# Optimization experiments

Hardware: AMD Instinct MI355X
Metric: run time of the kernel (lower is better)

## Reference

```python
import jax, jax.numpy as jnp
import numpy as np
from math import ceil

N, C_IN, HV, WV = 4, 3, 256, 256
C, K, NUM_LAYERS = 16, 3, 10
HK, WK = 45, 45
PROX_SCALE, KSCALE, KBSCALE, EPS = 10.0, 100.0, 0.01, 1e-8


def conv2_same(x, w):
    # torch F.conv2d (cross-correlation) with 'same' padding
    return jax.lax.conv_general_dilated(x, w, (1, 1), 'SAME',
                                        dimension_numbers=('NCHW', 'OIHW', 'NCHW'))


def pad_to(x, size):
    h, w = x.shape[-2], x.shape[-1]
    pads = [(0, 0)] * (x.ndim - 2) + [(0, size[0] - h), (0, size[1] - w)]
    return jnp.pad(x, pads)


def soft_threshold(x, b):
    return jnp.sign(x) * jax.nn.relu(jnp.abs(x) - b)


def circ_shift(x, s):
    return jnp.roll(x, (-s[0], -s[1]), axis=(-2, -1))


def csq(c):
    return (c * jnp.conj(c)).real


def forward(blurred_image, w0, ws, biases, kernel_biases, kernel_proxes, zetas, eta):
    Nb, C_in, Hv, Wv = blurred_image.shape
    Hs, Ws = Hv + HK - 1, Wv + WK - 1
    Hb, Wb = Hs + HK - 1, Ws + WK - 1
    fft_size = (int(ceil(Hb / 64.0) * 64), int(ceil(Wb / 64.0) * 64))
    rfft = lambda x: jnp.fft.rfft2(x, s=fft_size, axes=(-2, -1))
    irfft = lambda X: jnp.fft.irfft2(X, s=fft_size, axes=(-2, -1))

    # first-layer filter: zero-mean per (out,in) filter, then spatial reflect
    w_mean = w0.reshape(C, C_in, -1).mean(axis=-1)
    w0c = w0 - w_mean[:, :, None, None]
    w0_unreflected = jnp.transpose(w0c, (1, 0, 2, 3))   # (C_in, C, K, K)
    w0r = w0c[:, :, ::-1, ::-1]

    # analysis: cascade of convs, each feature stack padded to fft_size
    wy_list = []
    fy = blurred_image
    for layer in range(NUM_LAYERS):
        w = w0r if layer == 0 else ws[layer - 1]
        fy = conv2_same(fy, w)
        fy_p = pad_to(jnp.pad(fy, ((0, 0), (0, 0), (HK - 1, HK - 1), (WK - 1, WK - 1))), fft_size)
        wy_list.append(fy_p)

    delta = jnp.zeros((Nb, HK, WK), dtype=blurred_image.dtype).at[:, HK // 2, WK // 2].set(1.0)
    b0 = biases[0][None, :, None, None]
    z = soft_threshold(circ_shift(wy_list[-1], (HK // 2, WK // 2)), b0)
    Fz = rfft(z)
    k = delta
    Fg = None
    for layer in range(NUM_LAYERS):
        fy_p = wy_list.pop()
        Ffy = rfft(fy_p)                       # (N, C, H, Wf) complex
        Fk = rfft(k)[:, None]                  # (N, 1, H, Wf)
        zeta = PROX_SCALE * zetas[layer][None, :, None, None]
        num = zeta * (jnp.conj(Fk) * Ffy) + Fz
        den = zeta * csq(Fk) + 1.0
        Fg = num / (den + EPS)
        b = biases[layer + 1][None, :, None, None]
        z = soft_threshold(irfft(Fg), b)
        Fz = rfft(z)
        zk = kernel_proxes[layer]
        num_k = zk * jnp.sum(jnp.conj(Fz) * Ffy, axis=1) + Fk[:, 0]
        den_k = zk * jnp.sum(csq(Fz), axis=1) + 1.0
        k = irfft(num_k / (den_k + EPS))
        k_flat = k.reshape(Nb, -1)
        k_max = jax.scipy.special.logsumexp(k_flat * KSCALE, axis=-1) / KSCALE
        bk = KBSCALE * kernel_biases[layer]
        k = jax.nn.relu(k[:, :HK, :WK] - bk * k_max[:, None, None])
        k_sum = jnp.sum(k, axis=(1, 2), keepdims=True)
        k = (k + EPS * delta) / (k_sum + EPS)

    # final closed-form image solve in frequency domain (3-channel Cramer's rule)
    Fy = rfft(jnp.pad(blurred_image, ((0, 0), (0, 0), (HK - 1, HK - 1), (WK - 1, WK - 1))))
    Fk = rfft(k)                                # (N, H, Wf)
    Fw0 = rfft(circ_shift(pad_to(w0_unreflected, fft_size), (K // 2, K // 2)))  # (C_in, C, H, Wf)
    b_final = biases[NUM_LAYERS + 1][None, :, None, None]
    Fg = rfft(soft_threshold(irfft(Fg), b_final))

    eta_s = PROX_SCALE * eta[None, :, None, None]      # (1, C, 1, 1)
    Fwr, Fwg, Fwb = Fw0[0:1], Fw0[1:2], Fw0[2:3]       # (1, C, H, Wf)
    Fyr, Fyg, Fyb = Fy[:, 0], Fy[:, 1], Fy[:, 2]
    Fk_sq = csq(Fk)
    Crr = Fk_sq + jnp.sum(eta_s * csq(Fwr), axis=1)
    Cgg = Fk_sq + jnp.sum(eta_s * csq(Fwg), axis=1)
    Cbb = Fk_sq + jnp.sum(eta_s * csq(Fwb), axis=1)
    Crg = jnp.sum(eta_s * jnp.conj(Fwr) * Fwg, axis=1)
    Crb = jnp.sum(eta_s * jnp.conj(Fwr) * Fwb, axis=1)
    Cgb = jnp.sum(eta_s * jnp.conj(Fwg) * Fwb, axis=1)
    Fk_conj = jnp.conj(Fk)
    Br = Fk_conj * Fyr + jnp.sum(eta_s * jnp.conj(Fwr) * Fg, axis=1)
    Bg = Fk_conj * Fyg + jnp.sum(eta_s * jnp.conj(Fwg) * Fg, axis=1)
    Bb = Fk_conj * Fyb + jnp.sum(eta_s * jnp.conj(Fwb) * Fg, axis=1)
    Crg_sq, Crb_sq, Cgb_sq = csq(Crg), csq(Crb), csq(Cgb)
    Irr = Cgg * Cbb - Cgb_sq
    Igg = Crr * Cbb - Crb_sq
    Ibb = Crr * Cgg - Crg_sq
    Irg = jnp.conj(Cgb) * Crb - Cbb * Crg
    Irb = Crg * Cgb - Cgg * Crb
    Igb = jnp.conj(Crg) * Crb - Crr * Cgb
    den = (Crr * (Cgg * Cbb - Cgb_sq) - Cgg * Crb_sq - Cbb * Crg_sq
           + 2 * (Crg * Cgb * jnp.conj(Crb)).real) + EPS
    Fxr = Irr * Br + Irg * Bg + Irb * Bb
    Fxg = jnp.conj(Irg) * Br + Igg * Bg + Igb * Bb
    Fxb = jnp.conj(Irb) * Br + jnp.conj(Igb) * Bg + Ibb * Bb
    Fx = jnp.stack([Fxr, Fxg, Fxb], axis=1) / den[:, None]

    image = irfft(Fx)[:, :, HK // 2:HK // 2 + Hv, WK // 2:WK // 2 + Wv]
    return image, k


def setup_inputs() -> dict:
    key = jax.random.key(0)
    ks = jax.random.split(key, 4)

    def xavier(k, shape, fan_in, fan_out):
        std = (2.0 / (fan_in + fan_out)) ** 0.5
        return std * jax.random.normal(k, shape, dtype=jnp.float32)

    return {
        'blurred_image': jax.random.normal(ks[0], (N, C_IN, HV, WV), dtype=jnp.float32),
        'w0': xavier(ks[1], (C, C_IN, K, K), C_IN * K * K, C * K * K),
        'ws': xavier(ks[2], (NUM_LAYERS - 1, C, C, 3, 3), C * 9, C * 9),
        'biases': jnp.full((NUM_LAYERS + 2, C), 0.02, dtype=jnp.float32),
        'kernel_biases': jnp.zeros((NUM_LAYERS,), dtype=jnp.float32),
        'kernel_proxes': jnp.ones((NUM_LAYERS,), dtype=jnp.float32),
        'zetas': jnp.ones((NUM_LAYERS, C), dtype=jnp.float32),
        'eta': jnp.ones((C,), dtype=jnp.float32),
    }


def reference(blurred_image, w0, ws, biases, kernel_biases, kernel_proxes, zetas, eta):
    return forward(blurred_image, w0, ws, biases, kernel_biases, kernel_proxes, zetas, eta)
```

## Files before the change

kernel.cpp:

```cpp
#include <hip/hip_runtime.h>
#include <math.h>

#define FH 384
#define KF 193
#define KS 384
#define SPW 147456

typedef __attribute__((ext_vector_type(8))) short short8;
typedef __attribute__((ext_vector_type(4))) float f32x4;
typedef unsigned int u32;
typedef unsigned short u16;

static __device__ __forceinline__ float softt(float v, float b) {
    return copysignf(fmaxf(fabsf(v) - b, 0.f), v);
}
static __device__ __forceinline__ u16 bf16_rn(float v) {
    u32 u = __float_as_uint(v);
    u32 r = (u + 0x7FFFu + ((u >> 16) & 1u)) >> 16;
    return (u16)r;
}
static __device__ __forceinline__ float bf16_to_f(u16 h) {
    return __uint_as_float(((u32)h) << 16);
}
static __device__ __forceinline__ float2 ldc(const uint2* __restrict__ S, size_t i) {
    uint2 u = S[i];
    float2 r;
    r.x = __uint_as_float((u.x & 0xffffu) << 16) + __uint_as_float((u.y & 0xffffu) << 16);
    r.y = __uint_as_float(u.x & 0xffff0000u) + __uint_as_float(u.y & 0xffff0000u);
    return r;
}
static __device__ __forceinline__ uint2 packc(float re, float im) {
    u16 hr = bf16_rn(re), hi = bf16_rn(im);
    u16 lr = bf16_rn(re - bf16_to_f(hr)), li = bf16_rn(im - bf16_to_f(hi));
    uint2 o; o.x = (u32)hr | ((u32)hi << 16); o.y = (u32)lr | ((u32)li << 16);
    return o;
}

__global__ void init_ef_k(float2* Ef) {
    int idx = blockIdx.x * 256 + threadIdx.x;
    if (idx >= FH * FH) return;
    int h = idx / FH, j = idx % FH;
    int m = (h * j) % FH;
    float th = (float)(6.283185307179586 / FH) * (float)m;
    float2 v; v.x = cosf(th); v.y = -sinf(th);
    Ef[idx] = v;
}

__global__ void init_tw(float2* twT) {
    int i = blockIdx.x * 256 + threadIdx.x;
    if (i < 193) {
        float th = (float)(6.283185307179586 / 384.0) * (float)i;
        float2 v; v.x = cosf(th); v.y = sinf(th);
        twT[i] = v;
    }
}

__global__ void init_estack192(u16* __restrict__ H, u16* __restrict__ L, int inv)
{
    int idx = blockIdx.x * 256 + threadIdx.x;
    if (idx >= KS * KS) return;
    int gm = idx / KS, kp = idx % KS;
    int m = gm >> 1, comp = gm & 1;
    int t = kp >> 1, ri = kp & 1;
    int mm = (m * t) % 192;
    float th = (float)(6.283185307179586 / 192.0) * (float)mm;
    float c = cosf(th), s = sinf(th);
    float er, ei;
    if (inv) { er = c * (1.f/384.f); ei = s * (1.f/384.f); }
    else     { er = c;               ei = -s; }
    float v;
    if (comp == 0) v = (ri == 0) ? er : -ei;
    else           v = (ri == 0) ? ei :  er;
    u16 h = bf16_rn(v);
    H[idx] = h;
    L[idx] = bf16_rn(v - bf16_to_f(h));
}

__global__ void init_t192(u16* __restrict__ H, u16* __restrict__ L)
{
    int idx = blockIdx.x * 256 + threadIdx.x;
    if (idx >= 208 * 192) return;
    int n = idx / 192, m = idx % 192;
    float v = 0.f;
    if (n < 194) {
        int j = n >> 1, ri = n & 1;
        int mm = (j * m) % 192;
        float th = (float)(6.283185307179586 / 192.0) * (float)mm;
        v = ri ? -sinf(th) : cosf(th);
    }
    u16 h = bf16_rn(v);
    H[idx] = h;
    L[idx] = bf16_rn(v - bf16_to_f(h));
}

__global__ void init_u192(u16* __restrict__ H, u16* __restrict__ L)
{
    int idx = blockIdx.x * 256 + threadIdx.x;
    if (idx >= 192 * 224) return;
    int m = idx / 224, kk = idx % 224;
    float v = 0.f;
    if (kk < 194) {
        int j = kk >> 1, ri = kk & 1;
        float cj = (j == 0 || j == 96) ? (1.f/384.f) : (2.f/384.f);
        int mm = (j * m) % 192;
        float th = (float)(6.283185307179586 / 192.0) * (float)mm;
        v = ri ? -cj*sinf(th) : cj*cosf(th);
    }
    u16 h = bf16_rn(v);
// ... 249 lines not shown
#pragma unroll
    for (int mi = 0; mi < 2; ++mi)
#pragma unroll
        for (int nj = 0; nj < 4; ++nj) {
            accA[mi][nj] = (f32x4){0.f,0.f,0.f,0.f};
            accB[mi][nj] = (f32x4){0.f,0.f,0.f,0.f};
        }
    const u16* hP = Hs + (size_t)plane*inH*inW;
    const u16* lP = Ls + (size_t)plane*inH*inW;
    int W2  = inW >> 1;
    int ox2 = offX >> 1;
    bool al16 = ((ox2 & 7) == 0);
    int mhi = (offX + inW) >> 1;
    for (int kt = 0; kt < mhi; kt += 32) {
#pragma unroll
        for (int s = 0; s < 4; ++s) {
            int slot = tid + s*256;
            int p    = slot >> 9;
            int inr  = slot & 511;
            int r = inr >> 2, kq2 = inr & 3;
            int yy = y0 + r - offY;
            int m0 = kt + kq2*8;
            int pos = m0 - ox2;
            uint4 hq = {0u,0u,0u,0u}, lq4 = {0u,0u,0u,0u};
            if (yy >= 0 && yy < inH) {
                const u16* hr = hP + (size_t)yy*inW + (size_t)p*W2;
                const u16* lr = lP + (size_t)yy*inW + (size_t)p*W2;
                if (pos >= 0 && pos + 8 <= W2) {
                    if (al16) {
                        hq  = *(const uint4*)(hr + pos);
                        lq4 = *(const uint4*)(lr + pos);
                    } else {
                        hq.x = *(const u32*)(hr+pos);   hq.y = *(const u32*)(hr+pos+2);
                        hq.z = *(const u32*)(hr+pos+4); hq.w = *(const u32*)(hr+pos+6);
                        lq4.x = *(const u32*)(lr+pos);   lq4.y = *(const u32*)(lr+pos+2);
                        lq4.z = *(const u32*)(lr+pos+4); lq4.w = *(const u32*)(lr+pos+6);
                    }
                } else if (pos + 8 > 0 && pos < W2) {
#pragma unroll
                    for (int q = 0; q < 4; ++q) {
                        int pp = pos + 2*q;
                        if (pp >= 0 && pp + 2 <= W2) {
                            ((u32*)&hq)[q]  = *(const u32*)(hr+pp);
                            ((u32*)&lq4)[q] = *(const u32*)(lr+pp);
                        }
                    }
                }
            }
            int base = ((r >> 4)*64 + (r & 15) + 16*kq2)*8;
            *(uint4*)&AhS[p][base] = hq;
            *(uint4*)&AlS[p][base] = lq4;
        }
        __syncthreads();
        short8 A0h[2], A0l[2], A1h[2], A1l[2];
#pragma unroll
        for (int mi = 0; mi < 2; ++mi) {
            int fo = ((wave*2 + mi)*64 + lane)*8;
            A0h[mi] = *(const short8*)&AhS[0][fo];
            A0l[mi] = *(const short8*)&AlS[0][fo];
            A1h[mi] = *(const short8*)&AhS[1][fo];
            A1l[mi] = *(const short8*)&AlS[1][fo];
        }
#pragma unroll
        for (int nj = 0; nj < 4; ++nj) {
            if (nj >= njN) continue;
            size_t toff = (size_t)(col0 + nj*16 + lm)*192 + kt + lq*8;
            short8 Bh = *(const short8*)(TH + toff);
            short8 Bl = *(const short8*)(TL + toff);
#pragma unroll
            for (int mi = 0; mi < 2; ++mi) {
                accA[mi][nj] = __builtin_amdgcn_mfma_f32_16x16x32_bf16(A0h[mi], Bh, accA[mi][nj], 0, 0, 0);
                accA[mi][nj] = __builtin_amdgcn_mfma_f32_16x16x32_bf16(A0h[mi], Bl, accA[mi][nj], 0, 0, 0);
                accA[mi][nj] = __builtin_amdgcn_mfma_f32_16x16x32_bf16(A0l[mi], Bh, accA[mi][nj], 0, 0, 0);
                accB[mi][nj] = __builtin_amdgcn_mfma_f32_16x16x32_bf16(A1h[mi], Bh, accB[mi][nj], 0, 0, 0);
                accB[mi][nj] = __builtin_amdgcn_mfma_f32_16x16x32_bf16(A1h[mi], Bl, accB[mi][nj], 0, 0, 0);
                accB[mi][nj] = __builtin_amdgcn_mfma_f32_16x16x32_bf16(A1l[mi], Bh, accB[mi][nj], 0, 0, 0);
            }
        }
        __syncthreads();
    }
    r2c192_epilogue(accA, accB, col0, njN, y0, wave, lm, lq, twT, outp, B, plane);
}

__global__ void gpm_kernel(uint2* __restrict__ S, const float2* __restrict__ twT, int rows)
{
    int idx = blockIdx.x*256 + threadIdx.x;
    if (idx >= rows * 97) return;
    int j = idx % 97;
    size_t b = (size_t)(idx / 97) * KF;
    if (j == 96) {
        float2 f = ldc(S, b + 96);
        S[b + 96] = packc(2.f*f.x, -2.f*f.y);
    } else {
        float2 f1 = ldc(S, b + j);
        float2 f2 = ldc(S, b + 192 - j);
        float gpx = f1.x + f2.x, gpy = f1.y - f2.y;
        float hx  = f1.x - f2.x, hy  = f1.y + f2.y;
        float2 tw = twT[j];
        float gmx = tw.x*hx - tw.y*hy;
        float gmy = tw.x*hy + tw.y*hx;
        S[b + j]       = packc(gpx, gpy);
        S[b + 192 - j] = packc(gmx, gmy);
    }
}

__global__ __launch_bounds__(256) void c2r192(
    const uint2* __restrict__ Ain,
    const u16* __restrict__ UH, const u16* __restrict__ UL,
    float* __restrict__ outp, const float* __restrict__ thr,
    u16* __restrict__ spH, u16* __restrict__ spL, int B)
{
    __shared__ u16 AhS[2][8*64*8];
    __shared__ u16 AlS[2][8*64*8];
    int col0 = blockIdx.x * 64;
    int y0   = blockIdx.y * 128;
    int plane = blockIdx.z;
    int tid = threadIdx.x;
    int wave = tid >> 6, lane = tid & 63;
    int lm = lane & 15, lq = lane >> 4;
    f32x4 accP[2][4], accQ[2][4];
#pragma unroll
    for (int mi = 0; mi < 2; ++mi)
#pragma unroll
        for (int nj = 0; nj < 4; ++nj) {
            accP[mi][nj] = (f32x4){0.f,0.f,0.f,0.f};
            accQ[mi][nj] = (f32x4){0.f,0.f,0.f,0.f};
        }
    for (int kt = 0; kt < 194; kt += 32) {
#pragma unroll
        for (int s = 0; s < 8; ++s) {
            int slot = tid + s*256;
            int p   = slot >> 10;
            int inr = slot & 1023;
            int r = inr >> 3, kq = inr & 7;
            size_t rowb = ((size_t)(y0 + r)*B + plane)*KF;
            int j0 = (kt + kq*4) >> 1;
            uint2 u0, u1;
            u0.x = u0.y = u1.x = u1.y = 0u;
            if (p == 0) {
                if (j0 < 96) u0 = Ain[rowb + j0];
                else if (j0 == 96) {
                    uint2 t = Ain[rowb + 96];
                    u0.x = t.x & 0xffffu; u0.y = t.y & 0xffffu;
                }
                if (j0 + 1 < 96) u1 = Ain[rowb + j0 + 1];
            } else {
                if (j0 < 96) u0 = Ain[rowb + 192 - j0];
                else if (j0 == 96) {
                    uint2 t = Ain[rowb + 96];
                    u0.x = t.x >> 16; u0.y = t.y >> 16;
                }
                if (j0 + 1 < 96) u1 = Ain[rowb + 191 - j0];
            }
            int base = ((r >> 4)*64 + (r & 15) + 16*(kq >> 1))*8 + (kq & 1)*4;
            uint2 hp, lp;
            hp.x = u0.x; hp.y = u1.x;
            lp.x = u0.y; lp.y = u1.y;
            *(uint2*)&AhS[p][base] = hp;
            *(uint2*)&AlS[p][base] = lp;
        }
        __syncthreads();
        short8 A0h[2], A0l[2], A1h[2], A1l[2];
#pragma unroll
        for (int mi = 0; mi < 2; ++mi) {
            int fo = ((wave*2 + mi)*64 + lane)*8;
            A0h[mi] = *(const short8*)&AhS[0][fo];
            A0l[mi] = *(const short8*)&AlS[0][fo];
            A1h[mi] = *(const short8*)&AhS[1][fo];
            A1l[mi] = *(const short8*)&AlS[1][fo];
        }
#pragma unroll
        for (int nj = 0; nj < 4; ++nj) {
            size_t toff = (size_t)(col0 + nj*16 + lm)*224 + kt + lq*8;
            short8 Bh = *(const short8*)(UH + toff);
            short8 Bl = *(const short8*)(UL + toff);
#pragma unroll
            for (int mi = 0; mi < 2; ++mi) {
                accP[mi][nj] = __builtin_amdgcn_mfma_f32_16x16x32_bf16(A0h[mi], Bh, accP[mi][nj], 0, 0, 0);
                accP[mi][nj] = __builtin_amdgcn_mfma_f32_16x16x32_bf16(A0h[mi], Bl, accP[mi][nj], 0, 0, 0);
                accP[mi][nj] = __builtin_amdgcn_mfma_f32_16x16x32_bf16(A0l[mi], Bh, accP[mi][nj], 0, 0, 0);
                accQ[mi][nj] = __builtin_amdgcn_mfma_f32_16x16x32_bf16(A1h[mi], Bh, accQ[mi][nj], 0, 0, 0);
                accQ[mi][nj] = __builtin_amdgcn_mfma_f32_16x16x32_bf16(A1h[mi], Bl, accQ[mi][nj], 0, 0, 0);
                accQ[mi][nj] = __builtin_amdgcn_mfma_f32_16x16x32_bf16(A1l[mi], Bh, accQ[mi][nj], 0, 0, 0);
            }
        }
        __syncthreads();
    }
    float bthr = thr ? thr[plane & 15] : 0.f;
#pragma unroll
    for (int mi = 0; mi < 2; ++mi) {
#pragma unroll
        for (int nj = 0; nj < 4; ++nj) {
            int m = col0 + nj*16 + lm;
#pragma unroll
            for (int rr = 0; rr < 4; ++rr) {
                int y = y0 + wave*32 + mi*16 + lq*4 + rr;
                float xe = accP[mi][nj][rr];
                float xo = accQ[mi][nj][rr];
                float2 o2; o2.x = xe; o2.y = xo;
                *(float2*)&outp[((size_t)plane*FH + y)*FH + 2*m] = o2;
                if (spH) {
                    float s0 = softt(xe, bthr), s1 = softt(xo, bthr);
                    u16 h0 = bf16_rn(s0), h1 = bf16_rn(s1);
                    u16 l0 = bf16_rn(s0 - bf16_to_f(h0)), l1 = bf16_rn(s1 - bf16_to_f(h1));
                    size_t d = (size_t)plane*SPW + (size_t)y*FH + m;
                    spH[d]       = h0; spL[d]       = l0;
                    spH[d + 192] = h1; spL[d + 192] = l1;
                }
            }
        }
    }
}

__global__ __launch_bounds__(256) void zgemm_col_mfma2(
    const u16* __restrict__ EH, const u16* __restrict__ EL,
    const uint2* __restrict__ Bm, uint2* __restrict__ Cm, int N, float sgn,
    int ktHi, const float2* __restrict__ twT)
{
    __shared__ u16 BhS[2][4*64*8];
    __shared__ u16 BlS[2][4*64*8];
    int col0 = blockIdx.x * 64;
    int row0 = blockIdx.y * 128;
    int tid = threadIdx.x;
    int wave = tid >> 6, lane = tid & 63;
    int lm = lane & 15, lq = lane >> 4;
    f32x4 accE[2][4], accO[2][4];
#pragma unroll
    for (int mi = 0; mi < 2; ++mi)
#pragma unroll
        for (int nj = 0; nj < 4; ++nj) {
            accE[mi][nj] = (f32x4){0.f,0.f,0.f,0.f};
            accO[mi][nj] = (f32x4){0.f,0.f,0.f,0.f};
        }
    int arow0 = row0 + wave*32 + lm;
    for (int kt = 0; kt < ktHi; kt += 32) {
        int tbase = kt >> 1;
#pragma unroll
        for (int s = 0; s < 4; ++s) {
            int slot = tid + s*256;
            int p    = slot >> 9;
            int inr  = slot & 511;
            int pair = inr >> 6;
            int n    = inr & 63;
            int gn   = col0 + n;
            int t0   = tbase + pair*2;
            uint2 u0, u1;
            u0.x = u0.y = u1.x = u1.y = 0u;
            if (gn < N) {
                u0 = Bm[(size_t)(2*t0 + p)*N + gn];
                u1 = Bm[(size_t)(2*t0 + 2 + p)*N + gn];
            }
            int ntile = n >> 4, n0 = n & 15;
            int lrow  = (pair >> 1)*16 + n0;
            int base  = (ntile*64 + lrow)*8 + (pair & 1)*4;
            uint2 hp, lp;
            hp.x = u0.x; hp.y = u1.x;
            lp.x = u0.y; lp.y = u1.y;
            *(uint2*)&BhS[p][base] = hp;
            *(uint2*)&BlS[p][base] = lp;
        }
        __syncthreads();
        short8 Ah[2], Al[2];
#pragma unroll
        for (int mi = 0; mi < 2; ++mi) {
            size_t aoff = (size_t)(arow0 + mi*16)*KS + kt + lq*8;
            Ah[mi] = *(const short8*)(EH + aoff);
            Al[mi] = *(const short8*)(EL + aoff);
        }
#pragma unroll
        for (int nj = 0; nj < 4; ++nj) {
            short8 Bh0 = *(const short8*)&BhS[0][(nj*64 + lane)*8];
            short8 Bl0 = *(const short8*)&BlS[0][(nj*64 + lane)*8];
            short8 Bh1 = *(const short8*)&BhS[1][(nj*64 + lane)*8];
            short8 Bl1 = *(const short8*)&BlS[1][(nj*64 + lane)*8];
#pragma unroll
            for (int mi = 0; mi < 2; ++mi) {
                accE[mi][nj] = __builtin_amdgcn_mfma_f32_16x16x32_bf16(Ah[mi], Bh0, accE[mi][nj], 0, 0, 0);
                accE[mi][nj] = __builtin_amdgcn_mfma_f32_16x16x32_bf16(Ah[mi], Bl0, accE[mi][nj], 0, 0, 0);
                accE[mi][nj] = __builtin_amdgcn_mfma_f32_16x16x32_bf16(Al[mi], Bh0, accE[mi][nj], 0, 0, 0);
                accO[mi][nj] = __builtin_amdgcn_mfma_f32_16x16x32_bf16(Ah[mi], Bh1, accO[mi][nj], 0, 0, 0);
                accO[mi][nj] = __builtin_amdgcn_mfma_f32_16x16x32_bf16(Ah[mi], Bl1, accO[mi][nj], 0, 0, 0);
                accO[mi][nj] = __builtin_amdgcn_mfma_f32_16x16x32_bf16(Al[mi], Bh1, accO[mi][nj], 0, 0, 0);
            }
        }
        __syncthreads();
    }
#pragma unroll
    for (int mi = 0; mi < 2; ++mi) {
#pragma unroll
        for (int nj = 0; nj < 4; ++nj) {
            int coln = col0 + nj*16 + lm;
            if (coln < N) {
                int r0 = row0 + wave*32 + mi*16 + lq*4;
                int h  = r0 >> 1;
#pragma unroll
                for (int pp = 0; pp < 2; ++pp) {
                    float e_re = accE[mi][nj][2*pp],   e_im = accE[mi][nj][2*pp+1];
                    float o_re = accO[mi][nj][2*pp],   o_im = accO[mi][nj][2*pp+1];
                    int hh = h + pp;
                    float2 tw = twT[hh];
                    float twr = tw.x, twi = sgn * tw.y;
                    float tr = twr*o_re - twi*o_im;
                    float ti = twr*o_im + twi*o_re;
                    Cm[(size_t)hh*N + coln]         = packc(e_re + tr, e_im + ti);
                    Cm[(size_t)(hh + 192)*N + coln] = packc(e_re - tr, e_im - ti);
                }
            }
        }
    }
}

__global__ void fg_kernel(const uint2* __restrict__ Ffy, uint2* __restrict__ Fz,
                          const uint2* __restrict__ Fk, const float* __restrict__ zetas,
                          int L, int total)
{
    int idx = blockIdx.x*256 + threadIdx.x;
    if (idx >= total) return;
    int k = idx % KF; int r = idx / KF;
    int c = r & 15; int hi = r >> 4;
    float zeta = 10.f * zetas[L*16 + c];
    float2 fk = ldc(Fk, (size_t)hi*KF + k);
    float2 fy = ldc(Ffy, idx);
    float2 fz = ldc(Fz, idx);
    float nx = zeta*(fk.x*fy.x + fk.y*fy.y) + fz.x;
    float ny = zeta*(fk.x*fy.y - fk.y*fy.x) + fz.y;
    float den = zeta*(fk.x*fk.x + fk.y*fk.y) + 1.f + 1e-8f;
    float inv = 1.f/den;
    Fz[idx] = packc(nx*inv, ny*inv);
}

__global__ void knum_kernel(const uint2* __restrict__ Fz, const uint2* __restrict__ Ffy,
                            const uint2* __restrict__ Fk, const float* __restrict__ kprox,
                            int L, int total, uint2* __restrict__ outk)
{
    int idx = blockIdx.x*256 + threadIdx.x;
    if (idx >= total) return;
    int k = idx % KF; int r = idx / KF;
    float zk = kprox[L];
    float s1x = 0.f, s1y = 0.f, s2 = 0.f;
    for (int c = 0; c < 16; ++c) {
        size_t bi = ((size_t)r*16 + c)*KF + k;
        float2 fz = ldc(Fz, bi), fy = ldc(Ffy, bi);
        s1x += fz.x*fy.x + fz.y*fy.y;
        s1y += fz.x*fy.y - fz.y*fy.x;
        s2  += fz.x*fz.x + fz.y*fz.y;
    }
    float2 fk = ldc(Fk, idx);
    float nx = zk*s1x + fk.x, ny = zk*s1y + fk.y;
    float den = zk*s2 + 1.f + 1e-8f;
    float inv = 1.f/den;
    outk[idx] = packc(nx*inv, ny*inv);
}

__device__ __forceinline__ void lse_comb(float& m, float& s, float m2, float s2)
{
    if (m2 > m) { s = s * expf(m - m2) + s2; m = m2; }
    else        { s = s + s2 * expf(m2 - m); }
}

__global__ __launch_bounds__(256) void lse_part_kernel(const float* __restrict__ kraw0,
                                                       float2* __restrict__ parts)
{
    int img = blockIdx.y;
    const float* kraw = kraw0 + (size_t)img*FH*FH;
    int b = blockIdx.x, t = threadIdx.x;
    float m = -1e30f, s = 0.f;
    for (int i = b*256 + t; i < FH*FH; i += 64*256) {
        float v = 100.f * kraw[i];
        lse_comb(m, s, v, 1.f);
    }
    __shared__ float sm[256], ss[256];
    sm[t] = m; ss[t] = s;
    __syncthreads();
    for (int st = 128; st > 0; st >>= 1) {
        if (t < st) {
            float mm = sm[t], sc = ss[t];
            lse_comb(mm, sc, sm[t+st], ss[t+st]);
            sm[t] = mm; ss[t] = sc;
        }
        __syncthreads();
    }
    if (t == 0) { float2 o; o.x = sm[0]; o.y = ss[0]; parts[img*64 + b] = o; }
}

__global__ void zero_kernel(float* __restrict__ p, int n)
{
    int i = blockIdx.x*256 + threadIdx.x;
    if (i < n) p[i] = 0.f;
}

__global__ void kdelta_kernel(float* __restrict__ kful, int G)
{
    int t = threadIdx.x;
    if (t < G) kful[(size_t)t*FH*FH + 22*FH + 22] = 1.f;
}

__global__ __launch_bounds__(256) void knew_kernel(const float2* __restrict__ parts,
    const float* __restrict__ kraw0, const float* __restrict__ kb, int L,
    float* __restrict__ kful0)
{
    int img = blockIdx.x;
    const float* kraw = kraw0 + (size_t)img*FH*FH;
    float*       kful = kful0 + (size_t)img*FH*FH;
    int t = threadIdx.x;
    __shared__ float sm[64], ss[64];
    if (t < 64) { float2 p = parts[img*64 + t]; sm[t] = p.x; ss[t] = p.y; }
    __syncthreads();
    for (int st = 32; st > 0; st >>= 1) {
        if (t < st) {
            float mm = sm[t], sc = ss[t];
            lse_comb(mm, sc, sm[t+st], ss[t+st]);
            sm[t] = mm; ss[t] = sc;
        }
        __syncthreads();
    }
    float kmax = (sm[0] + logf(ss[0])) * 0.01f;
    float thr = 0.01f * kb[L] * kmax;
    float vs[8]; float loc = 0.f;
#pragma unroll
    for (int ii = 0; ii < 8; ++ii) {
        int i = t + ii*256;
        float v = 0.f;
        if (i < 45*45) {
            int y = i/45, x = i - y*45;
            v = fmaxf(kraw[y*FH + x] - thr, 0.f);
        }
        vs[ii] = v; loc += v;
    }
    __shared__ float sr[256];
    sr[t] = loc; __syncthreads();
    for (int st = 128; st > 0; st >>= 1) { if (t < st) sr[t] += sr[t+st]; __syncthreads(); }
    float den = sr[0] + 1e-8f;
#pragma unroll
    for (int ii = 0; ii < 8; ++ii) {
        int i = t + ii*256;
        if (i < 45*45) {
            int y = i/45, x = i - y*45;
            float v = vs[ii] + ((y == 22 && x == 22) ? 1e-8f : 0.f);
            kful[y*FH + x] = v / den;
        }
    }
}

__global__ void fw0_kernel(const float* __restrict__ w0c, const float2* __restrict__ Ef,
                           float2* __restrict__ Fw0)
{
    int idx = blockIdx.x*256 + threadIdx.x;
    if (idx >= 48*FH*KF) return;
    int k = idx % KF; int r = idx / KF;
    int c = r & 15; int r2 = r >> 4;
    int ci = r2 % 3; int h = r2 / 3;
    float accx = 0.f, accy = 0.f;
#pragma unroll
    for (int ky = 0; ky < 3; ++ky) {
        int a1 = ky - 1; if (a1 < 0) a1 += FH;
        float2 e1 = Ef[h*FH + a1];
#pragma unroll
        for (int kx = 0; kx < 3; ++kx) {
            int a2 = kx - 1; if (a2 < 0) a2 += FH;
            float2 e2 = Ef[k*FH + a2];
            float wv = w0c[((c*3 + ci)*3 + ky)*3 + kx];
            float tr = e1.x*e2.x - e1.y*e2.y;
            float ti = e1.x*e2.y + e1.y*e2.x;
            accx += wv*tr; accy += wv*ti;
        }
    }
    float2 o; o.x = accx; o.y = accy;
    Fw0[idx] = o;
}

__global__ void wiener_kernel(const uint2* __restrict__ Fk, const uint2* __restrict__ Fy,
    const float2* __restrict__ Fw0, const uint2* __restrict__ Fg2,
    const float* __restrict__ eta, int G, int total, uint2* __restrict__ Fx)
{
    int idx = blockIdx.x*256 + threadIdx.x;
    if (idx >= total) return;
    int k = idx % KF; int r = idx / KF;
    int h = r / G;
    float2 fk = ldc(Fk, idx);
    float fksq = fk.x*fk.x + fk.y*fk.y;
    float2 fyr = ldc(Fy, ((size_t)3*r + 0)*KF + k);
    float2 fyg = ldc(Fy, ((size_t)3*r + 1)*KF + k);
    float2 fyb = ldc(Fy, ((size_t)3*r + 2)*KF + k);
    float Crr = fksq, Cgg = fksq, Cbb = fksq;
    float2 Crg, Crb, Cgb;
    Crg.x = Crg.y = Crb.x = Crb.y = Cgb.x = Cgb.y = 0.f;
    float2 Br, Bg, Bb;
    Br.x = fk.x*fyr.x + fk.y*fyr.y; Br.y = fk.x*fyr.y - fk.y*fyr.x;
    Bg.x = fk.x*fyg.x + fk.y*fyg.y; Bg.y = fk.x*fyg.y - fk.y*fyg.x;
    Bb.x = fk.x*fyb.x + fk.y*fyb.y; Bb.y = fk.x*fyb.y - fk.y*fyb.x;
    for (int c = 0; c < 16; ++c) {
// ... 61 lines not shown
extern "C" void kernel_launch(void* const* d_in, const int* in_sizes, int n_in,
                              void* d_out, int out_size, void* d_ws, size_t ws_size,
                              hipStream_t stream)
{
    (void)in_sizes; (void)n_in; (void)out_size;
    const float* blurred = (const float*)d_in[0];
    const float* w0      = (const float*)d_in[1];
    const float* wsw     = (const float*)d_in[2];
    const float* biases  = (const float*)d_in[3];
    const float* kbias   = (const float*)d_in[4];
    const float* kprox   = (const float*)d_in[5];
    const float* zetas   = (const float*)d_in[6];
    const float* eta     = (const float*)d_in[7];
    float* outp = (float*)d_out;

    auto al = [](size_t b) { return (b + 255) & ~(size_t)255; };
    auto need = [&](int G) -> size_t {
        size_t s = 0;
        s += al((size_t)FH*FH*8);
        s += al(193*8);
        s += 4*al((size_t)KS*KS*2);
        s += 2*al((size_t)208*192*2);
        s += 2*al((size_t)192*224*2);
        s += al(432*4);
        s += 2*al((size_t)10*G*16*65536*2);
        s += al((size_t)G*16*FH*FH*4);
        s += 2*al((size_t)G*16*SPW*2);
        s += 3*al((size_t)G*16*FH*KF*8);
        s += 3*al((size_t)G*FH*KF*8);
        s += 2*al((size_t)G*FH*FH*4);
        s += 2*al((size_t)G*3*FH*KF*8);
        s += al((size_t)G*64*8);
        return s;
    };
    int G = 4;
    while (G > 1 && need(G) > ws_size) G >>= 1;

    char* base = (char*)d_ws;
    size_t off = 0;
    auto alloc = [&](size_t bytes) -> void* {
        void* p = (void*)(base + off);
        off += (bytes + 255) & ~(size_t)255;
        return p;
    };
    float2* Ef   = (float2*)alloc((size_t)FH*FH*8);
    float2* twT  = (float2*)alloc(193*8);
    u16* EfH = (u16*)alloc((size_t)KS*KS*2);
    u16* EfL = (u16*)alloc((size_t)KS*KS*2);
    u16* EiH = (u16*)alloc((size_t)KS*KS*2);
    u16* EiL = (u16*)alloc((size_t)KS*KS*2);
    u16* T1H = (u16*)alloc((size_t)208*192*2);
    u16* T1L = (u16*)alloc((size_t)208*192*2);
    u16* U1H = (u16*)alloc((size_t)192*224*2);
    u16* U1L = (u16*)alloc((size_t)192*224*2);
    float*  w0cB = (float*)alloc(432*4);
    u16*    fyH  = (u16*)alloc((size_t)10*G*16*65536*2);
    u16*    fyL  = (u16*)alloc((size_t)10*G*16*65536*2);
    float*  zsp  = (float*)alloc((size_t)G*16*FH*FH*4);
    u16*    zspSH= (u16*)alloc((size_t)G*16*SPW*2);
    u16*    zspSL= (u16*)alloc((size_t)G*16*SPW*2);
    uint2*  mid  = (uint2*)alloc((size_t)G*16*FH*KF*8);
    uint2*  FzFg = (uint2*)alloc((size_t)G*16*FH*KF*8);
    uint2*  Ffy  = (uint2*)alloc((size_t)G*16*FH*KF*8);
    uint2*  Fk   = (uint2*)alloc((size_t)G*FH*KF*8);
    uint2*  kfA  = (uint2*)alloc((size_t)G*FH*KF*8);
    uint2*  kfB  = (uint2*)alloc((size_t)G*FH*KF*8);
    float*  kraw = (float*)alloc((size_t)G*FH*FH*4);
    float*  kful = (float*)alloc((size_t)G*FH*FH*4);
    uint2*  FyB  = (uint2*)alloc((size_t)G*3*FH*KF*8);
    uint2*  FxB  = (uint2*)alloc((size_t)G*3*FH*KF*8);
    float2* lseP = (float2*)alloc((size_t)G*64*8);
    float2* Fw0B = (float2*)fyH;

    init_ef_k<<<(FH*FH+255)/256, 256, 0, stream>>>(Ef);
    init_tw<<<1, 256, 0, stream>>>(twT);
    init_estack192<<<(KS*KS+255)/256, 256, 0, stream>>>(EfH, EfL, 0);
    init_estack192<<<(KS*KS+255)/256, 256, 0, stream>>>(EiH, EiL, 1);
    init_t192<<<(208*192+255)/256, 256, 0, stream>>>(T1H, T1L);
    init_u192<<<(192*224+255)/256, 256, 0, stream>>>(U1H, U1L);
    w0c_kernel<<<1, 64, 0, stream>>>(w0, w0cB);

    auto zgf = [&](const uint2* Bm, uint2* Cm, int Ncols) {
        zgemm_col_mfma2<<<dim3((Ncols+63)/64, 3), 256, 0, stream>>>(
            EfH, EfL, Bm, Cm, Ncols, -1.f, KS, twT);
    };
    auto zgi = [&](const uint2* Bm, uint2* Cm, int Ncols) {
        zgemm_col_mfma2<<<dim3((Ncols+63)/64, 3), 256, 0, stream>>>(
            EiH, EiL, Bm, Cm, Ncols, 1.f, KS, twT);
    };
    auto r2c = [&](const float* inp, int inH, int inW, int oY, int oX,
                   const float* thr, uint2* o, int B) {
        r2c192_f<<<dim3(4, 3, B), 256, 0, stream>>>(
            inp, inH, inW, inW, (size_t)inH*inW, oY, oX, thr, T1H, T1L, twT, o, B);
    };
    auto r2cs = [&](const u16* Hs, const u16* Ls, int inH, int inW, int oY, int oX,
                    uint2* o, int B) {
        r2c192_s<<<dim3(4, 3, B), 256, 0, stream>>>(
            Hs, Ls, inH, inW, oY, oX, T1H, T1L, twT, o, B);
    };
    auto c2r = [&](uint2* Ain, float* o, int B,
                   const float* thr, u16* sH, u16* sL) {
        int rows = FH * B;
        gpm_kernel<<<(rows*97 + 255)/256, 256, 0, stream>>>(Ain, twT, rows);
        c2r192<<<dim3(3, 3, B), 256, 0, stream>>>(
            Ain, U1H, U1L, o, thr, sH, sL, B);
    };
    auto r2ck = [&]() {
        r2c192_f<<<dim3(4, 1, G), 256, 0, stream>>>(
            kful, 45, 45, FH, (size_t)FH*FH, 0, 0, nullptr, T1H, T1L, twT, mid, G);
        zgemm_col_mfma2<<<dim3((G*KF+63)/64, 3), 256, 0, stream>>>(
            EfH, EfL, mid, Fk, G*KF, -1.f, 64, twT);
    };

    const size_t CKL = (size_t)G*16*65536;

    for (int g0 = 0; g0 < 4; g0 += G) {
        const float* img = blurred + (size_t)g0*3*65536;

        conv3x3_kernel<<<dim3(16,16,G), 256, 0, stream>>>(
            img, nullptr, nullptr, w0cB, fyH, fyL, 3, 1, (size_t)3*65536);
        for (int l = 1; l < 10; ++l)
            conv3x3_kernel<<<dim3(16,16,G), 256, 0, stream>>>(
                nullptr, fyH + (size_t)(l-1)*CKL, fyL + (size_t)(l-1)*CKL,
                wsw + (size_t)(l-1)*2304,
                fyH + (size_t)l*CKL, fyL + (size_t)l*CKL, 16, 0, (size_t)16*65536);

        int totZ = G*16*FH*FH;
        zinit_kernel<<<(totZ+255)/256, 256, 0, stream>>>(
            fyH + 9*CKL, fyL + 9*CKL, biases, zspSH, zspSL, totZ);
        r2cs(zspSH, zspSL, FH, FH, 0, 0, mid, G*16);
        zgf(mid, FzFg, G*16*KF);

        zero_kernel<<<(G*FH*FH+255)/256, 256, 0, stream>>>(kful, G*FH*FH);
        kdelta_kernel<<<1, 64, 0, stream>>>(kful, G);

        int totS = G*16*FH*KF;
        int totK = G*FH*KF;
        for (int it = 0; it < 10; ++it) {
            int Lfy = 9 - it;
            r2cs(fyH + (size_t)Lfy*CKL, fyL + (size_t)Lfy*CKL, 256, 256, 44, 44, mid, G*16);
            zgf(mid, Ffy, G*16*KF);
            r2ck();
            fg_kernel<<<(totS+255)/256, 256, 0, stream>>>(Ffy, FzFg, Fk, zetas, it, totS);
            zgi(FzFg, mid, G*16*KF);
            c2r(mid, zsp, G*16, biases + (it+1)*16, zspSH, zspSL);
            r2cs(zspSH, zspSL, FH, FH, 0, 0, mid, G*16);
            zgf(mid, FzFg, G*16*KF);
            knum_kernel<<<(totK+255)/256, 256, 0, stream>>>(FzFg, Ffy, Fk, kprox, it, totK, kfA);
            zgi(kfA, kfB, G*KF);
            c2r(kfB, kraw, G, nullptr, nullptr, nullptr);
            lse_part_kernel<<<dim3(64,G), 256, 0, stream>>>(kraw, lseP);
            knew_kernel<<<G, 256, 0, stream>>>(lseP, kraw, kbias, it, kful);
        }

        r2c(img, 256, 256, 44, 44, nullptr, mid, 3*G);
        zgf(mid, FyB, 3*G*KF);
        r2ck();
        r2c(zsp, FH, FH, 0, 0, biases + 11*16, mid, G*16);
        zgf(mid, FzFg, G*16*KF);
        fw0_kernel<<<(48*FH*KF+255)/256, 256, 0, stream>>>(w0cB, Ef, Fw0B);
        wiener_kernel<<<(totK+255)/256, 256, 0, stream>>>(Fk, FyB, Fw0B, FzFg, eta, G, totK, FxB);
        zgi(FxB, mid, 3*G*KF);
        c2r(mid, zsp, 3*G, nullptr, nullptr, nullptr);
        int totC = G*3*65536;
        crop_kernel<<<(totC+255)/256, 256, 0, stream>>>(zsp, outp + (size_t)g0*3*65536, totC);
        int totKC = G*2025;
        kcopy_kernel<<<(totKC+255)/256, 256, 0, stream>>>(kful, outp + 786432 + g0*2025, totKC);
    }
}
```

Baseline: 8.726 ms.

## Fuse pre-twiddle, Fg update and LSE partials into FFT GEMM kernels

Folds the gpm pre-processing (even/odd split with twiddles) into the c2r192 tile loader, fuses the fg_kernel update into the inverse column GEMM's B-tile load, and computes log-sum-exp partials in the c2r epilogue instead of a separate pass. This removes three standalone memory-bound kernels per iteration and their extra global reads and writes. In exchange, the loaders do more arithmetic and redundant loads (each c2r block recomputes its pair values), and the LSE partial count changes from 64 to 9 per image.

```diff
diff --git a/kernel.cpp b/kernel.cpp
--- a/kernel.cpp
+++ b/kernel.cpp
@@ -24,6 +24,12 @@
 }
 static __device__ __forceinline__ float2 ldc(const uint2* __restrict__ S, size_t i) {
     uint2 u = S[i];
+    float2 r;
+    r.x = __uint_as_float((u.x & 0xffffu) << 16) + __uint_as_float((u.y & 0xffffu) << 16);
+    r.y = __uint_as_float(u.x & 0xffff0000u) + __uint_as_float(u.y & 0xffff0000u);
+    return r;
+}
+static __device__ __forceinline__ float2 ldcu(uint2 u) {
     float2 r;
     r.x = __uint_as_float((u.x & 0xffffu) << 16) + __uint_as_float((u.y & 0xffffu) << 16);
     r.y = __uint_as_float(u.x & 0xffff0000u) + __uint_as_float(u.y & 0xffff0000u);
@@ -439,33 +445,19 @@
     r2c192_epilogue(accA, accB, col0, njN, y0, wave, lm, lq, twT, outp, B, plane);
 }
 
-__global__ void gpm_kernel(uint2* __restrict__ S, const float2* __restrict__ twT, int rows)
-{
-    int idx = blockIdx.x*256 + threadIdx.x;
-    if (idx >= rows * 97) return;
-    int j = idx % 97;
-    size_t b = (size_t)(idx / 97) * KF;
-    if (j == 96) {
-        float2 f = ldc(S, b + 96);
-        S[b + 96] = packc(2.f*f.x, -2.f*f.y);
-    } else {
-        float2 f1 = ldc(S, b + j);
-        float2 f2 = ldc(S, b + 192 - j);
-        float gpx = f1.x + f2.x, gpy = f1.y - f2.y;
-        float hx  = f1.x - f2.x, hy  = f1.y + f2.y;
-        float2 tw = twT[j];
-        float gmx = tw.x*hx - tw.y*hy;
-        float gmy = tw.x*hy + tw.y*hx;
-        S[b + j]       = packc(gpx, gpy);
-        S[b + 192 - j] = packc(gmx, gmy);
-    }
+__device__ __forceinline__ void lse_comb(float& m, float& s, float m2, float s2)
+{
+    if (m2 > m) { s = s * expf(m - m2) + s2; m = m2; }
+    else        { s = s + s2 * expf(m2 - m); }
 }
 
 __global__ __launch_bounds__(256) void c2r192(
     const uint2* __restrict__ Ain,
     const u16* __restrict__ UH, const u16* __restrict__ UL,
+    const float2* __restrict__ twT,
     float* __restrict__ outp, const float* __restrict__ thr,
-    u16* __restrict__ spH, u16* __restrict__ spL, int B)
+    u16* __restrict__ spH, u16* __restrict__ spL, int B,
+    float2* __restrict__ parts)
 {
     __shared__ u16 AhS[2][8*64*8];
     __shared__ u16 AlS[2][8*64*8];
@@ -485,36 +477,44 @@
         }
     for (int kt = 0; kt < 194; kt += 32) {
 #pragma unroll
-        for (int s = 0; s < 8; ++s) {
+        for (int s = 0; s < 4; ++s) {
             int slot = tid + s*256;
-            int p   = slot >> 10;
-            int inr = slot & 1023;
-            int r = inr >> 3, kq = inr & 7;
+            int r = slot >> 3, kq = slot & 7;
             size_t rowb = ((size_t)(y0 + r)*B + plane)*KF;
             int j0 = (kt + kq*4) >> 1;
-            uint2 u0, u1;
-            u0.x = u0.y = u1.x = u1.y = 0u;
-            if (p == 0) {
-                if (j0 < 96) u0 = Ain[rowb + j0];
-                else if (j0 == 96) {
-                    uint2 t = Ain[rowb + 96];
-                    u0.x = t.x & 0xffffu; u0.y = t.y & 0xffffu;
-                }
-                if (j0 + 1 < 96) u1 = Ain[rowb + j0 + 1];
-            } else {
-                if (j0 < 96) u0 = Ain[rowb + 192 - j0];
-                else if (j0 == 96) {
-                    uint2 t = Ain[rowb + 96];
-                    u0.x = t.x >> 16; u0.y = t.y >> 16;
-                }
-                if (j0 + 1 < 96) u1 = Ain[rowb + 191 - j0];
-            }
+            int j1 = j0 + 1;
+            float2 gp0 = {0.f,0.f}, gm0 = {0.f,0.f};
+            float2 gp1 = {0.f,0.f}, gm1 = {0.f,0.f};
+            if (j0 < 96) {
+                float2 f1 = ldc(Ain, rowb + j0);
+                float2 f2 = ldc(Ain, rowb + 192 - j0);
+                gp0.x = f1.x + f2.x; gp0.y = f1.y - f2.y;
+                float hx = f1.x - f2.x, hy = f1.y + f2.y;
+                float2 tw = twT[j0];
+                gm0.x = tw.x*hx - tw.y*hy;
+                gm0.y = tw.x*hy + tw.y*hx;
+            } else if (j0 == 96) {
+                float2 f = ldc(Ain, rowb + 96);
+                gp0.x = 2.f*f.x;
+                gm0.x = -2.f*f.y;
+            }
+            if (j1 < 96) {
+                float2 f1 = ldc(Ain, rowb + j1);
+                float2 f2 = ldc(Ain, rowb + 192 - j1);
+                gp1.x = f1.x + f2.x; gp1.y = f1.y - f2.y;
+                float hx = f1.x - f2.x, hy = f1.y + f2.y;
+                float2 tw = twT[j1];
+                gm1.x = tw.x*hx - tw.y*hy;
+                gm1.y = tw.x*hy + tw.y*hx;
+            }
+            uint2 e0 = packc(gp0.x, gp0.y), e1 = packc(gp1.x, gp1.y);
+            uint2 o0 = packc(gm0.x, gm0.y), o1 = packc(gm1.x, gm1.y);
             int base = ((r >> 4)*64 + (r & 15) + 16*(kq >> 1))*8 + (kq & 1)*4;
-            uint2 hp, lp;
-            hp.x = u0.x; hp.y = u1.x;
-            lp.x = u0.y; lp.y = u1.y;
-            *(uint2*)&AhS[p][base] = hp;
-            *(uint2*)&AlS[p][base] = lp;
+            uint2 w;
+            w.x = e0.x; w.y = e1.x; *(uint2*)&AhS[0][base] = w;
+            w.x = e0.y; w.y = e1.y; *(uint2*)&AlS[0][base] = w;
+            w.x = o0.x; w.y = o1.x; *(uint2*)&AhS[1][base] = w;
+            w.x = o0.y; w.y = o1.y; *(uint2*)&AlS[1][base] = w;
         }
         __syncthreads();
         short8 A0h[2], A0l[2], A1h[2], A1l[2];
@@ -544,6 +544,7 @@
         __syncthreads();
     }
     float bthr = thr ? thr[plane & 15] : 0.f;
+    float lm_ = -1e30f, ls_ = 0.f;
 #pragma unroll
     for (int mi = 0; mi < 2; ++mi) {
 #pragma unroll
@@ -564,7 +565,28 @@
                     spH[d]       = h0; spL[d]       = l0;
                     spH[d + 192] = h1; spL[d + 192] = l1;
                 }
-            }
+                if (parts) {
+                    lse_comb(lm_, ls_, 100.f*xe, 1.f);
+                    lse_comb(lm_, ls_, 100.f*xo, 1.f);
+                }
+            }
+        }
+    }
+    if (parts) {
+        __shared__ float sm[256], ss[256];
+        sm[tid] = lm_; ss[tid] = ls_;
+        __syncthreads();
+        for (int st = 128; st > 0; st >>= 1) {
+            if (tid < st) {
+                float mm = sm[tid], sc = ss[tid];
+                lse_comb(mm, sc, sm[tid+st], ss[tid+st]);
+                sm[tid] = mm; ss[tid] = sc;
+            }
+            __syncthreads();
+        }
+        if (tid == 0) {
+            float2 o; o.x = sm[0]; o.y = ss[0];
+            parts[plane*9 + blockIdx.y*3 + blockIdx.x] = o;
         }
     }
 }
@@ -572,7 +594,9 @@
 __global__ __launch_bounds__(256) void zgemm_col_mfma2(
     const u16* __restrict__ EH, const u16* __restrict__ EL,
     const uint2* __restrict__ Bm, uint2* __restrict__ Cm, int N, float sgn,
-    int ktHi, const float2* __restrict__ twT)
+    int ktHi, const float2* __restrict__ twT,
+    const uint2* __restrict__ Ffy, const uint2* __restrict__ FkB,
+    const float* __restrict__ zet16, int GKF)
 {
     __shared__ u16 BhS[2][4*64*8];
     __shared__ u16 BlS[2][4*64*8];
@@ -581,6 +605,28 @@
     int tid = threadIdx.x;
     int wave = tid >> 6, lane = tid & 63;
     int lm = lane & 15, lq = lane >> 4;
+    const bool fuse = (Ffy != nullptr);
+    int p_[4], pair_[4], gn_[4], imgk_[4];
+    float zeta_[4];
+    bool ok_[4];
+#pragma unroll
+    for (int s = 0; s < 4; ++s) {
+        int slot = tid + s*256;
+        p_[s]    = slot >> 9;
+        int inr  = slot & 511;
+        pair_[s] = inr >> 6;
+        int n    = inr & 63;
+        int gn   = col0 + n;
+        gn_[s]   = gn;
+        ok_[s]   = (gn < N);
+        imgk_[s] = 0; zeta_[s] = 0.f;
+        if (fuse && ok_[s]) {
+            int plane = gn / KF;
+            int k = gn - plane*KF;
+            imgk_[s] = (plane >> 4)*KF + k;
+            zeta_[s] = 10.f * zet16[plane & 15];
+        }
+    }
     f32x4 accE[2][4], accO[2][4];
 #pragma unroll
     for (int mi = 0; mi < 2; ++mi)
@@ -594,19 +640,32 @@
         int tbase = kt >> 1;
 #pragma unroll
         for (int s = 0; s < 4; ++s) {
-            int slot = tid + s*256;
-            int p    = slot >> 9;
-            int inr  = slot & 511;
-            int pair = inr >> 6;
-            int n    = inr & 63;
-            int gn   = col0 + n;
-            int t0   = tbase + pair*2;
+            int p = p_[s], pair = pair_[s], gn = gn_[s];
+            int t0 = tbase + pair*2;
+            int ua = 2*t0 + p;
             uint2 u0, u1;
             u0.x = u0.y = u1.x = u1.y = 0u;
-            if (gn < N) {
-                u0 = Bm[(size_t)(2*t0 + p)*N + gn];
-                u1 = Bm[(size_t)(2*t0 + 2 + p)*N + gn];
-            }
+            if (ok_[s]) {
+                u0 = Bm[(size_t)ua*N + gn];
+                u1 = Bm[(size_t)(ua+2)*N + gn];
+                if (fuse) {
+                    float zeta = zeta_[s];
+#pragma unroll
+                    for (int e = 0; e < 2; ++e) {
+                        int u = ua + 2*e;
+                        float2 fz = ldcu(e ? u1 : u0);
+                        float2 fy = ldc(Ffy, (size_t)u*N + gn);
+                        float2 fk = ldc(FkB, (size_t)u*GKF + imgk_[s]);
+                        float nx = zeta*(fk.x*fy.x + fk.y*fy.y) + fz.x;
+                        float ny = zeta*(fk.x*fy.y - fk.y*fy.x) + fz.y;
+                        float den = zeta*(fk.x*fk.x + fk.y*fk.y) + 1.f + 1e-8f;
+                        float inv = 1.f/den;
+                        uint2 r = packc(nx*inv, ny*inv);
+                        if (e) u1 = r; else u0 = r;
+                    }
+                }
+            }
+            int n = gn - col0;
             int ntile = n >> 4, n0 = n & 15;
             int lrow  = (pair >> 1)*16 + n0;
             int base  = (ntile*64 + lrow)*8 + (pair & 1)*4;
@@ -667,25 +726,6 @@
     }
 }
 
-__global__ void fg_kernel(const uint2* __restrict__ Ffy, uint2* __restrict__ Fz,
-                          const uint2* __restrict__ Fk, const float* __restrict__ zetas,
-                          int L, int total)
-{
-    int idx = blockIdx.x*256 + threadIdx.x;
-    if (idx >= total) return;
-    int k = idx % KF; int r = idx / KF;
-    int c = r & 15; int hi = r >> 4;
-    float zeta = 10.f * zetas[L*16 + c];
-    float2 fk = ldc(Fk, (size_t)hi*KF + k);
-    float2 fy = ldc(Ffy, idx);
-    float2 fz = ldc(Fz, idx);
-    float nx = zeta*(fk.x*fy.x + fk.y*fy.y) + fz.x;
-    float ny = zeta*(fk.x*fy.y - fk.y*fy.x) + fz.y;
-    float den = zeta*(fk.x*fk.x + fk.y*fk.y) + 1.f + 1e-8f;
-    float inv = 1.f/den;
-    Fz[idx] = packc(nx*inv, ny*inv);
-}
-
 __global__ void knum_kernel(const uint2* __restrict__ Fz, const uint2* __restrict__ Ffy,
                             const uint2* __restrict__ Fk, const float* __restrict__ kprox,
                             int L, int total, uint2* __restrict__ outk)
@@ -709,37 +749,6 @@
     outk[idx] = packc(nx*inv, ny*inv);
 }
 
-__device__ __forceinline__ void lse_comb(float& m, float& s, float m2, float s2)
-{
-    if (m2 > m) { s = s * expf(m - m2) + s2; m = m2; }
-    else        { s = s + s2 * expf(m2 - m); }
-}
-
-__global__ __launch_bounds__(256) void lse_part_kernel(const float* __restrict__ kraw0,
-                                                       float2* __restrict__ parts)
-{
-    int img = blockIdx.y;
-    const float* kraw = kraw0 + (size_t)img*FH*FH;
-    int b = blockIdx.x, t = threadIdx.x;
-    float m = -1e30f, s = 0.f;
-    for (int i = b*256 + t; i < FH*FH; i += 64*256) {
-        float v = 100.f * kraw[i];
-        lse_comb(m, s, v, 1.f);
-    }
-    __shared__ float sm[256], ss[256];
-    sm[t] = m; ss[t] = s;
-    __syncthreads();
-    for (int st = 128; st > 0; st >>= 1) {
-        if (t < st) {
-            float mm = sm[t], sc = ss[t];
-            lse_comb(mm, sc, sm[t+st], ss[t+st]);
-            sm[t] = mm; ss[t] = sc;
-        }
-        __syncthreads();
-    }
-    if (t == 0) { float2 o; o.x = sm[0]; o.y = ss[0]; parts[img*64 + b] = o; }
-}
-
 __global__ void zero_kernel(float* __restrict__ p, int n)
 {
     int i = blockIdx.x*256 + threadIdx.x;
@@ -760,10 +769,13 @@
     const float* kraw = kraw0 + (size_t)img*FH*FH;
     float*       kful = kful0 + (size_t)img*FH*FH;
     int t = threadIdx.x;
-    __shared__ float sm[64], ss[64];
-    if (t < 64) { float2 p = parts[img*64 + t]; sm[t] = p.x; ss[t] = p.y; }
+    __shared__ float sm[16], ss[16];
+    if (t < 16) {
+        if (t < 9) { float2 p = parts[img*9 + t]; sm[t] = p.x; ss[t] = p.y; }
+        else       { sm[t] = -1e30f; ss[t] = 0.f; }
+    }
     __syncthreads();
-    for (int st = 32; st > 0; st >>= 1) {
+    for (int st = 8; st > 0; st >>= 1) {
         if (t < st) {
             float mm = sm[t], sc = ss[t];
             lse_comb(mm, sc, sm[t+st], ss[t+st]);
@@ -991,11 +1003,11 @@
 
     auto zgf = [&](const uint2* Bm, uint2* Cm, int Ncols) {
         zgemm_col_mfma2<<<dim3((Ncols+63)/64, 3), 256, 0, stream>>>(
-            EfH, EfL, Bm, Cm, Ncols, -1.f, KS, twT);
+            EfH, EfL, Bm, Cm, Ncols, -1.f, KS, twT, nullptr, nullptr, nullptr, 0);
     };
     auto zgi = [&](const uint2* Bm, uint2* Cm, int Ncols) {
         zgemm_col_mfma2<<<dim3((Ncols+63)/64, 3), 256, 0, stream>>>(
-            EiH, EiL, Bm, Cm, Ncols, 1.f, KS, twT);
+            EiH, EiL, Bm, Cm, Ncols, 1.f, KS, twT, nullptr, nullptr, nullptr, 0);
     };
     auto r2c = [&](const float* inp, int inH, int inW, int oY, int oX,
                    const float* thr, uint2* o, int B) {
@@ -1007,18 +1019,16 @@
         r2c192_s<<<dim3(4, 3, B), 256, 0, stream>>>(
             Hs, Ls, inH, inW, oY, oX, T1H, T1L, twT, o, B);
     };
-    auto c2r = [&](uint2* Ain, float* o, int B,
-                   const float* thr, u16* sH, u16* sL) {
-        int rows = FH * B;
-        gpm_kernel<<<(rows*97 + 255)/256, 256, 0, stream>>>(Ain, twT, rows);
+    auto c2r = [&](const uint2* Ain, float* o, int B,
+                   const float* thr, u16* sH, u16* sL, float2* parts) {
         c2r192<<<dim3(3, 3, B), 256, 0, stream>>>(
-            Ain, U1H, U1L, o, thr, sH, sL, B);
+            Ain, U1H, U1L, twT, o, thr, sH, sL, B, parts);
     };
     auto r2ck = [&]() {
         r2c192_f<<<dim3(4, 1, G), 256, 0, stream>>>(
             kful, 45, 45, FH, (size_t)FH*FH, 0, 0, nullptr, T1H, T1L, twT, mid, G);
         zgemm_col_mfma2<<<dim3((G*KF+63)/64, 3), 256, 0, stream>>>(
-            EfH, EfL, mid, Fk, G*KF, -1.f, 64, twT);
+            EfH, EfL, mid, Fk, G*KF, -1.f, 64, twT, nullptr, nullptr, nullptr, 0);
     };
 
     const size_t CKL = (size_t)G*16*65536;
@@ -1043,22 +1053,22 @@
         zero_kernel<<<(G*FH*FH+255)/256, 256, 0, stream>>>(kful, G*FH*FH);
         kdelta_kernel<<<1, 64, 0, stream>>>(kful, G);
 
-        int totS = G*16*FH*KF;
         int totK = G*FH*KF;
+        int NS = G*16*KF;
         for (int it = 0; it < 10; ++it) {
             int Lfy = 9 - it;
             r2cs(fyH + (size_t)Lfy*CKL, fyL + (size_t)Lfy*CKL, 256, 256, 44, 44, mid, G*16);
             zgf(mid, Ffy, G*16*KF);
             r2ck();
-            fg_kernel<<<(totS+255)/256, 256, 0, stream>>>(Ffy, FzFg, Fk, zetas, it, totS);
-            zgi(FzFg, mid, G*16*KF);
-            c2r(mid, zsp, G*16, biases + (it+1)*16, zspSH, zspSL);
+            zgemm_col_mfma2<<<dim3((NS+63)/64, 3), 256, 0, stream>>>(
+                EiH, EiL, FzFg, mid, NS, 1.f, KS, twT,
+                Ffy, Fk, zetas + it*16, G*KF);
+            c2r(mid, zsp, G*16, biases + (it+1)*16, zspSH, zspSL, nullptr);
             r2cs(zspSH, zspSL, FH, FH, 0, 0, mid, G*16);
             zgf(mid, FzFg, G*16*KF);
             knum_kernel<<<(totK+255)/256, 256, 0, stream>>>(FzFg, Ffy, Fk, kprox, it, totK, kfA);
             zgi(kfA, kfB, G*KF);
-            c2r(kfB, kraw, G, nullptr, nullptr, nullptr);
-            lse_part_kernel<<<dim3(64,G), 256, 0, stream>>>(kraw, lseP);
+            c2r(kfB, kraw, G, nullptr, nullptr, nullptr, lseP);
             knew_kernel<<<G, 256, 0, stream>>>(lseP, kraw, kbias, it, kful);
         }
 
@@ -1070,7 +1080,7 @@
         fw0_kernel<<<(48*FH*KF+255)/256, 256, 0, stream>>>(w0cB, Ef, Fw0B);
         wiener_kernel<<<(totK+255)/256, 256, 0, stream>>>(Fk, FyB, Fw0B, FzFg, eta, G, totK, FxB);
         zgi(FxB, mid, 3*G*KF);
-        c2r(mid, zsp, 3*G, nullptr, nullptr, nullptr);
+        c2r(mid, zsp, 3*G, nullptr, nullptr, nullptr, nullptr);
         int totC = G*3*65536;
         crop_kernel<<<(totC+255)/256, 256, 0, stream>>>(zsp, outp + (size_t)g0*3*65536, totC);
         int totKC = G*2025;
```

Measured after the change: 9.638 ms. 10.5% more time.
